# Optimization experiments

Hardware: AMD Instinct MI355X
Metric: run time of the kernel (lower is better)

## Reference

```python
import jax, jax.numpy as jnp
import numpy as np

N_EXPERTS, D_IN, D_OUT = 8, 1024, 1024
N_TOKENS = 8192


def setup_inputs() -> dict:
    key = jax.random.key(0)
    ks = jax.random.split(key, 5)
    s_in = 1.0 / np.sqrt(D_IN)
    x = jax.random.normal(ks[0], (N_TOKENS, D_IN), dtype=jnp.float32)
    W = jax.random.uniform(ks[1], (N_EXPERTS, D_IN, D_OUT), jnp.float32, -s_in, s_in)
    b = jax.random.uniform(ks[2], (N_EXPERTS, D_OUT), jnp.float32, -s_in, s_in)
    gate_W = jax.random.uniform(ks[3], (D_IN, N_EXPERTS), jnp.float32, -s_in, s_in)
    gate_b = jax.random.uniform(ks[4], (N_EXPERTS,), jnp.float32, -s_in, s_in)
    return {"x": x, "W": W, "b": b, "gate_W": gate_W, "gate_b": gate_b}


def reference(x, W, b, gate_W, gate_b):
    # gate: [n, e] softmax over experts
    gate_score = jax.nn.softmax(x @ gate_W + gate_b, axis=-1)
    # all experts applied densely: [n, e, o]
    expert_outputs = jnp.einsum('ni,eio->neo', x, W) + b[None, :, :]
    # weighted combine over expert axis: [n, o]
    return jnp.einsum('ne,neo->no', gate_score, expert_outputs)
```

## Files before the change

### kernel.cpp

```cpp
#include <hip/hip_runtime.h>
#include <hip/hip_bf16.h>
#include <cstdint>
#include <cstddef>

#define N_TOK 8192
#define D_IN  1024
#define D_OUT 1024
#define N_EXP 8
#define KTOT  (N_EXP * D_IN)

typedef __attribute__((ext_vector_type(8))) short short8;
typedef __attribute__((ext_vector_type(8))) unsigned short ushort8;
typedef __attribute__((ext_vector_type(4))) float f32x4;

__device__ __forceinline__ unsigned short f2bf(float f) {
    union { float f; unsigned int u; } v; v.f = f;
    return (unsigned short)((v.u + 0x7FFFu + ((v.u >> 16) & 1u)) >> 16);
}

__device__ __forceinline__ void load_lds16(const void* g, void* l) {
    __builtin_amdgcn_global_load_lds(
        (const __attribute__((address_space(1))) void*)g,
        (__attribute__((address_space(3))) void*)l,
        16, 0, 0);
}

__global__ __launch_bounds__(256) void prep_kernel(
    const float* __restrict__ x, const float* __restrict__ gW,
    const float* __restrict__ gbias, const float* __restrict__ W,
    unsigned short* __restrict__ xb, unsigned short* __restrict__ Wt,
    float* __restrict__ g_t) {
    const int b = blockIdx.x;
    const int t = threadIdx.x;

    if (b < 2048) {
        __shared__ float tile[64][65];
        const int e  = b >> 8;
        const int i0 = ((b >> 4) & 15) * 64;
        const int o0 = (b & 15) * 64;

        const int rr = t >> 4;
        const int rc = (t & 15) * 4;
#pragma unroll
        for (int j = 0; j < 4; ++j) {
            const float4 v = *(const float4*)(
                W + ((size_t)e * D_IN + (i0 + rr + 16 * j)) * D_OUT + o0 + rc);
            tile[rr + 16 * j][rc + 0] = v.x;
            tile[rr + 16 * j][rc + 1] = v.y;
            tile[rr + 16 * j][rc + 2] = v.z;
            tile[rr + 16 * j][rc + 3] = v.w;
        }
        __syncthreads();
        const int ow = t >> 2;
        const int c  = (t & 3) * 16;
        ushort8 v0, v1;
#pragma unroll
        for (int j = 0; j < 8; ++j) v0[j] = f2bf(tile[c + j][ow]);
#pragma unroll
        for (int j = 0; j < 8; ++j) v1[j] = f2bf(tile[c + 8 + j][ow]);
        unsigned short* dst = Wt + (size_t)(o0 + ow) * KTOT + e * D_IN + i0 + c;
        *(ushort8*)dst = v0;
        *(ushort8*)(dst + 8) = v1;
    } else {
        const int lane = t & 63;
        const int n    = (b - 2048) * 4 + (t >> 6);

        float acc[8];
#pragma unroll
        for (int e = 0; e < 8; ++e) acc[e] = 0.f;
#pragma unroll
        for (int jj = 0; jj < 4; ++jj) {
            const int i = 256 * jj + 4 * lane;
            const float4 xv = *(const float4*)(x + (size_t)n * D_IN + i);
            ushort4 u;
            u.x = f2bf(xv.x); u.y = f2bf(xv.y);
            u.z = f2bf(xv.z); u.w = f2bf(xv.w);
            *(ushort4*)(xb + (size_t)n * D_IN + i) = u;
            const float xs[4] = {xv.x, xv.y, xv.z, xv.w};
#pragma unroll
            for (int j = 0; j < 4; ++j) {
                const float* wr = gW + (size_t)(i + j) * N_EXP;
                const float4 w0 = *(const float4*)wr;
                const float4 w1 = *(const float4*)(wr + 4);
                acc[0] += xs[j] * w0.x; acc[1] += xs[j] * w0.y;
                acc[2] += xs[j] * w0.z; acc[3] += xs[j] * w0.w;
                acc[4] += xs[j] * w1.x; acc[5] += xs[j] * w1.y;
                acc[6] += xs[j] * w1.z; acc[7] += xs[j] * w1.w;
            }
        }
#pragma unroll
        for (int off = 32; off > 0; off >>= 1) {
#pragma unroll
            for (int e = 0; e < 8; ++e) acc[e] += __shfl_down(acc[e], off);
        }
        if (lane == 0) {
            float lg[8], mx = -1e30f;
#pragma unroll
            for (int e = 0; e < 8; ++e) {
                lg[e] = acc[e] + gbias[e];
                mx = fmaxf(mx, lg[e]);
            }
            float s = 0.f;
#pragma unroll
            for (int e = 0; e < 8; ++e) { lg[e] = expf(lg[e] - mx); s += lg[e]; }
            const float inv = 1.f / s;
#pragma unroll
            for (int e = 0; e < 8; ++e)
                g_t[(size_t)e * N_TOK + n] = lg[e] * inv;
        }
    }
}

__global__ __launch_bounds__(256, 2) void moe_gemm4_kernel(
    const unsigned short* __restrict__ xb,
    const unsigned short* __restrict__ Wt,
    const float* __restrict__ bias,
    const float* __restrict__ g_t,
    float* __restrict__ out) {
    __shared__ __align__(16) unsigned short Abuf[2][128 * 32];
    __shared__ __align__(16) unsigned short Bbuf[2][128 * 32];
    __shared__ __align__(16) float g_s[N_EXP][128];
    __shared__ __align__(16) float r_s[N_EXP][128];
    __shared__ __align__(16) float b_s[N_EXP][128];

    const int t    = threadIdx.x;
    const int lane = t & 63;
    const int ln15 = lane & 15;
    const int quad = lane >> 4;
    const int wave = t >> 6;
    const int wm0  = (wave >> 1) * 64;
    const int wn0  = (wave & 1) * 64;
    const int bm0  = blockIdx.y * 128;
    const int bn0  = blockIdx.x * 128;

    for (int j = t; j < N_EXP * 128; j += 256) {
        const int e = j >> 7, r = j & 127;
        g_s[e][r] = g_t[(size_t)e * N_TOK + bm0 + r];
        b_s[e][r] = bias[(size_t)e * D_OUT + bn0 + r];
    }
    __syncthreads();
    if (t < 128) {
        float d[N_EXP];
#pragma unroll
        for (int e = 0; e < N_EXP; ++e) d[e] = fmaxf(g_s[e][t], 1e-30f);
#pragma unroll
        for (int e = 1; e < N_EXP; ++e) r_s[e][t] = d[e - 1] / d[e];
        r_s[0][t] = d[N_EXP - 1];
    }

    f32x4 acc[4][4];
#pragma unroll
    for (int mi = 0; mi < 4; ++mi)
#pragma unroll
        for (int ni = 0; ni < 4; ++ni)
            acc[mi][ni] = (f32x4){0.f, 0.f, 0.f, 0.f};

    unsigned short* aL0[2] = {&Abuf[0][wave * 512], &Abuf[1][wave * 512]};
    unsigned short* aL1[2] = {&Abuf[0][2048 + wave * 512], &Abuf[1][2048 + wave * 512]};
    unsigned short* bL0[2] = {&Bbuf[0][wave * 512], &Bbuf[1][wave * 512]};
    unsigned short* bL1[2] = {&Bbuf[0][2048 + wave * 512], &Bbuf[1][2048 + wave * 512]};

    const unsigned short* ga =
        xb + (size_t)(bm0 + (t >> 2)) * D_IN + (t & 3) * 8;
    const unsigned short* gbB =
        Wt + (size_t)(bn0 + (t >> 2)) * KTOT + (t & 3) * 8;

    __syncthreads();

    for (int e = 0; e < N_EXP; ++e) {
        if (e) {
#pragma unroll
            for (int mi = 0; mi < 4; ++mi) {
                const f32x4 rv = *(const f32x4*)&r_s[e][wm0 + mi * 16 + quad * 4];
#pragma unroll
                for (int ni = 0; ni < 4; ++ni)
#pragma unroll
                    for (int r = 0; r < 4; ++r) acc[mi][ni][r] *= rv[r];
            }
        }
        const unsigned short* gbe = gbB + (size_t)e * D_IN;

        for (int kk = 0; kk < 32; kk += 2) {
            __syncthreads();
            load_lds16(ga + kk * 32,                    aL0[0]);
            load_lds16(ga + 64 * D_IN + kk * 32,        aL1[0]);
            load_lds16(gbe + kk * 32,                   bL0[0]);
            load_lds16(gbe + 64 * KTOT + kk * 32,       bL1[0]);
            load_lds16(ga + (kk + 1) * 32,              aL0[1]);
            load_lds16(ga + 64 * D_IN + (kk + 1) * 32,  aL1[1]);
            load_lds16(gbe + (kk + 1) * 32,             bL0[1]);
            load_lds16(gbe + 64 * KTOT + (kk + 1) * 32, bL1[1]);
            __syncthreads();

#pragma unroll
            for (int s = 0; s < 2; ++s) {
                short8 af[4], bv[4];
#pragma unroll
                for (int mi = 0; mi < 4; ++mi)
                    af[mi] = *(const short8*)
                        &Abuf[s][(wm0 + mi * 16 + ln15) * 32 + quad * 8];
#pragma unroll
                for (int ni = 0; ni < 4; ++ni)
                    bv[ni] = *(const short8*)
                        &Bbuf[s][(wn0 + ni * 16 + ln15) * 32 + quad * 8];
#pragma unroll
                for (int mi = 0; mi < 4; ++mi)
#pragma unroll
                    for (int ni = 0; ni < 4; ++ni)
                        acc[mi][ni] = __builtin_amdgcn_mfma_f32_16x16x32_bf16(
                            af[mi], bv[ni], acc[mi][ni], 0, 0, 0);
            }
        }
    }

#pragma unroll
    for (int mi = 0; mi < 4; ++mi) {
        const f32x4 fin = *(const f32x4*)&r_s[0][wm0 + mi * 16 + quad * 4];
#pragma unroll
        for (int ni = 0; ni < 4; ++ni)
#pragma unroll
            for (int r = 0; r < 4; ++r) acc[mi][ni][r] *= fin[r];
    }
#pragma unroll
    for (int e = 0; e < N_EXP; ++e) {
        f32x4 gv[4];
        float bv[4];
#pragma unroll
        for (int mi = 0; mi < 4; ++mi)
            gv[mi] = *(const f32x4*)&g_s[e][wm0 + mi * 16 + quad * 4];
#pragma unroll
        for (int ni = 0; ni < 4; ++ni) bv[ni] = b_s[e][wn0 + ni * 16 + ln15];
#pragma unroll
        for (int mi = 0; mi < 4; ++mi)
#pragma unroll
            for (int ni = 0; ni < 4; ++ni)
#pragma unroll
                for (int r = 0; r < 4; ++r)
                    acc[mi][ni][r] += gv[mi][r] * bv[ni];
    }

#pragma unroll
    for (int mi = 0; mi < 4; ++mi) {
#pragma unroll
        for (int ni = 0; ni < 4; ++ni) {
            const int col  = bn0 + wn0 + ni * 16 + ln15;
            const int row0 = bm0 + wm0 + mi * 16 + quad * 4;
#pragma unroll
            for (int r = 0; r < 4; ++r)
                out[(size_t)(row0 + r) * D_OUT + col] = acc[mi][ni][r];
        }
    }
}

extern "C" void kernel_launch(void* const* d_in, const int* in_sizes, int n_in,
                              void* d_out, int out_size, void* d_ws, size_t ws_size,
                              hipStream_t stream) {
    const float* x  = (const float*)d_in[0];
    const float* W  = (const float*)d_in[1];
    const float* b  = (const float*)d_in[2];
    const float* gW = (const float*)d_in[3];
    const float* gb = (const float*)d_in[4];
    float* out = (float*)d_out;

    unsigned short* xb  = (unsigned short*)d_ws;
    unsigned short* Wt  = xb + (size_t)N_TOK * D_IN;
    float*          g_t = (float*)(Wt + (size_t)D_OUT * KTOT);

    prep_kernel<<<4096, 256, 0, stream>>>(x, gW, gb, W, xb, Wt, g_t);
    moe_gemm4_kernel<<<dim3(D_OUT / 128, N_TOK / 128), 256, 0, stream>>>(
        xb, Wt, b, g_t, out);
}
```

Before: 282.6 us.

## Software-pipeline the fused K loop with prefetch and swizzle block order

Replaces the per-expert double loop, which loads two K-slices and then computes with two barriers per step, by one flat loop over all 256 K-tiles. Each iteration prefetches the next tile into the other LDS buffer while running MFMAs on the current one, with a single barrier per iteration. The aim is to hide global-to-LDS load latency behind compute and to halve barrier count. It also remaps block indices so that consecutively launched blocks share weight column tiles, which should improve L2 reuse. The last iteration issues a wasted wrap-around prefetch, and correctness depends on the barrier waiting for the asynchronous LDS loads to finish.

Result: no change. 282.9 us (+0.1%).

```diff
diff --git a/kernel.cpp b/kernel.cpp
--- a/kernel.cpp
+++ b/kernel.cpp
@@ -111,7 +111,7 @@
     }
 }
 
-__global__ __launch_bounds__(256, 2) void moe_gemm4_kernel(
+__global__ __launch_bounds__(256, 2) void moe_gemm5_kernel(
     const unsigned short* __restrict__ xb,
     const unsigned short* __restrict__ Wt,
     const float* __restrict__ bias,
@@ -130,8 +130,12 @@
     const int wave = t >> 6;
     const int wm0  = (wave >> 1) * 64;
     const int wn0  = (wave & 1) * 64;
-    const int bm0  = blockIdx.y * 128;
-    const int bn0  = blockIdx.x * 128;
+
+    const int flat = blockIdx.x + 8 * blockIdx.y;
+    const int xs_  = (flat >> 3) & 7;
+    const int ys_  = ((flat & 7) << 3) | (flat >> 6);
+    const int bn0  = xs_ * 128;
+    const int bm0  = ys_ * 128;
 
     for (int j = t; j < N_EXP * 128; j += 256) {
         const int e = j >> 7, r = j & 127;
@@ -156,19 +160,35 @@
             acc[mi][ni] = (f32x4){0.f, 0.f, 0.f, 0.f};
 
     unsigned short* aL0[2] = {&Abuf[0][wave * 512], &Abuf[1][wave * 512]};
-    unsigned short* aL1[2] = {&Abuf[0][2048 + wave * 512], &Abuf[1][2048 + wave * 512]};
+    unsigned short* aL1[2] = {&Abuf[0][2048 + wave * 512],
+                              &Abuf[1][2048 + wave * 512]};
     unsigned short* bL0[2] = {&Bbuf[0][wave * 512], &Bbuf[1][wave * 512]};
-    unsigned short* bL1[2] = {&Bbuf[0][2048 + wave * 512], &Bbuf[1][2048 + wave * 512]};
+    unsigned short* bL1[2] = {&Bbuf[0][2048 + wave * 512],
+                              &Bbuf[1][2048 + wave * 512]};
 
     const unsigned short* ga =
         xb + (size_t)(bm0 + (t >> 2)) * D_IN + (t & 3) * 8;
     const unsigned short* gbB =
         Wt + (size_t)(bn0 + (t >> 2)) * KTOT + (t & 3) * 8;
 
+    load_lds16(ga, aL0[0]);
+    load_lds16(ga + 64 * D_IN, aL1[0]);
+    load_lds16(gbB, bL0[0]);
+    load_lds16(gbB + 64 * KTOT, bL1[0]);
     __syncthreads();
 
-    for (int e = 0; e < N_EXP; ++e) {
-        if (e) {
+    for (int kt = 0; kt < 256; ++kt) {
+        const int cb  = kt & 1;
+        const int nb  = cb ^ 1;
+        const int kt1 = (kt + 1) & 255;
+
+        load_lds16(ga + (kt1 & 31) * 32,              aL0[nb]);
+        load_lds16(ga + 64 * D_IN + (kt1 & 31) * 32,  aL1[nb]);
+        load_lds16(gbB + kt1 * 32,                    bL0[nb]);
+        load_lds16(gbB + 64 * KTOT + kt1 * 32,        bL1[nb]);
+
+        if (kt && !(kt & 31)) {
+            const int e = kt >> 5;
 #pragma unroll
             for (int mi = 0; mi < 4; ++mi) {
                 const f32x4 rv = *(const f32x4*)&r_s[e][wm0 + mi * 16 + quad * 4];
@@ -178,39 +198,24 @@
                     for (int r = 0; r < 4; ++r) acc[mi][ni][r] *= rv[r];
             }
         }
-        const unsigned short* gbe = gbB + (size_t)e * D_IN;
-
-        for (int kk = 0; kk < 32; kk += 2) {
-            __syncthreads();
-            load_lds16(ga + kk * 32,                    aL0[0]);
-            load_lds16(ga + 64 * D_IN + kk * 32,        aL1[0]);
-            load_lds16(gbe + kk * 32,                   bL0[0]);
-            load_lds16(gbe + 64 * KTOT + kk * 32,       bL1[0]);
-            load_lds16(ga + (kk + 1) * 32,              aL0[1]);
-            load_lds16(ga + 64 * D_IN + (kk + 1) * 32,  aL1[1]);
-            load_lds16(gbe + (kk + 1) * 32,             bL0[1]);
-            load_lds16(gbe + 64 * KTOT + (kk + 1) * 32, bL1[1]);
-            __syncthreads();
-
-#pragma unroll
-            for (int s = 0; s < 2; ++s) {
-                short8 af[4], bv[4];
-#pragma unroll
-                for (int mi = 0; mi < 4; ++mi)
-                    af[mi] = *(const short8*)
-                        &Abuf[s][(wm0 + mi * 16 + ln15) * 32 + quad * 8];
-#pragma unroll
-                for (int ni = 0; ni < 4; ++ni)
-                    bv[ni] = *(const short8*)
-                        &Bbuf[s][(wn0 + ni * 16 + ln15) * 32 + quad * 8];
-#pragma unroll
-                for (int mi = 0; mi < 4; ++mi)
-#pragma unroll
-                    for (int ni = 0; ni < 4; ++ni)
-                        acc[mi][ni] = __builtin_amdgcn_mfma_f32_16x16x32_bf16(
-                            af[mi], bv[ni], acc[mi][ni], 0, 0, 0);
-            }
-        }
+
+        short8 af[4], bv[4];
+#pragma unroll
+        for (int mi = 0; mi < 4; ++mi)
+            af[mi] = *(const short8*)
+                &Abuf[cb][(wm0 + mi * 16 + ln15) * 32 + quad * 8];
+#pragma unroll
+        for (int ni = 0; ni < 4; ++ni)
+            bv[ni] = *(const short8*)
+                &Bbuf[cb][(wn0 + ni * 16 + ln15) * 32 + quad * 8];
+#pragma unroll
+        for (int mi = 0; mi < 4; ++mi)
+#pragma unroll
+            for (int ni = 0; ni < 4; ++ni)
+                acc[mi][ni] = __builtin_amdgcn_mfma_f32_16x16x32_bf16(
+                    af[mi], bv[ni], acc[mi][ni], 0, 0, 0);
+
+        __syncthreads();
     }
 
 #pragma unroll
@@ -267,6 +272,6 @@
     float*          g_t = (float*)(Wt + (size_t)D_OUT * KTOT);
 
     prep_kernel<<<4096, 256, 0, stream>>>(x, gW, gb, W, xb, Wt, g_t);
-    moe_gemm4_kernel<<<dim3(D_OUT / 128, N_TOK / 128), 256, 0, stream>>>(
+    moe_gemm5_kernel<<<dim3(D_OUT / 128, N_TOK / 128), 256, 0, stream>>>(
         xb, Wt, b, g_t, out);
 }
```
